# Performance work log

Measured on AMD Instinct MI355X. Metric: run time of the kernel, lower is better.

Reference implementation:

```python
import jax, jax.numpy as jnp
import numpy as np

B, N, D_IN, D_OUT, H = 4, 512, 1024, 1024, 16
HD = D_IN // H      # key head dim (FAISS k_features)
VD = D_OUT // H     # value head dim
MEM = 32768         # memory_size per head
IPQ = 8             # items_per_query
SCALE = HD ** -0.5


def setup_inputs() -> dict:
    key = jax.random.key(0)
    ks = jax.random.split(key, 9)
    s = 0.02
    return {
        "x": jax.random.normal(ks[0], (B, N, D_IN), jnp.float32),
        "Wq": jax.random.normal(ks[1], (D_IN, D_IN), jnp.float32) * s,
        "Wk": jax.random.normal(ks[2], (D_IN, D_IN), jnp.float32) * s,
        "Wv": jax.random.normal(ks[3], (D_OUT, D_IN), jnp.float32) * s,
        "Ww": jax.random.normal(ks[4], (D_OUT, D_IN), jnp.float32) * s,
        "Wo": jax.random.normal(ks[5], (D_OUT, D_OUT), jnp.float32) * s,
        "bo": jnp.zeros((D_OUT,), jnp.float32),
        "k_mem0": jax.random.normal(ks[6], (H, MEM, HD), jnp.float32) * s,
        "v_mem0": jax.random.normal(ks[7], (H, MEM, VD), jnp.float32) * s,
    }


def _attention(q, k, v, Wo, bo):
    # q: [b,n,D_IN], k: [b,m,D_IN], v: [b,m,D_OUT]
    b, n, _ = q.shape
    m = k.shape[1]
    qh = q.reshape(b, n, H, HD)
    kh = k.reshape(b, m, H, HD)
    vh = v.reshape(b, m, H, VD)
    sim = jnp.einsum("bihd,bjhd->bhij", qh, kh) * SCALE
    att = jax.nn.softmax(sim, axis=-1)
    out = jnp.einsum("bhij,bjhd->bihd", att, vh).reshape(b, n, H * VD)
    return out @ Wo.T + bo


def reference(x, Wq, Wk, Wv, Ww, Wo, bo, k_mem0, v_mem0):
    b, n, _ = x.shape
    q = x @ Wq.T          # [b,n,D_IN]
    k = x @ Wk.T          # [b,n,D_IN]
    v = x @ Wv.T          # [b,n,D_OUT]
    w = jax.nn.sigmoid(x @ Ww.T)

    a = _attention(q, k, v, Wo, bo)

    # per-head flat views: [h, b*n, hd]
    qh = q.reshape(b, n, H, HD).transpose(2, 0, 1, 3).reshape(H, b * n, HD)
    kh = k.reshape(b, n, H, HD).transpose(2, 0, 1, 3).reshape(H, b * n, HD)
    vh = v.reshape(b, n, H, VD).transpose(2, 0, 1, 3).reshape(H, b * n, VD)

    m_ins = b * n
    # FIFO insert: drop oldest m_ins rows, append new keys/values
    k_mem = jnp.concatenate([k_mem0[:, m_ins:], kh], axis=1)  # [h, MEM, HD]
    v_mem = jnp.concatenate([v_mem0[:, m_ins:], vh], axis=1)  # [h, MEM, VD]

    # exact inner-product search (IndexFlatIP), top IPQ per query, per head
    sims = jnp.einsum("hqd,hmd->hqm", qh, k_mem)               # [h, b*n, MEM]
    _, idx = jax.lax.top_k(sims, IPQ)                          # [h, b*n, IPQ]
    idx = idx.reshape(H, b * n * IPQ, 1)
    k_ret = jnp.take_along_axis(k_mem, idx, axis=1)            # [h, b*n*IPQ, HD]
    v_ret = jnp.take_along_axis(v_mem, idx, axis=1)            # [h, b*n*IPQ, VD]

    # 'h (b m) hd -> b m (h hd)' with m = n*IPQ
    k_m = k_ret.reshape(H, b, n * IPQ, HD).transpose(1, 2, 0, 3).reshape(b, n * IPQ, D_IN)
    v_m = v_ret.reshape(H, b, n * IPQ, VD).transpose(1, 2, 0, 3).reshape(b, n * IPQ, D_OUT)

    a_m = _attention(q, k_m, v_m, Wo, bo)
    return w * a + (1.0 - w) * a_m
```

## Files before the change

### kernel.cpp

```cpp
#include <hip/hip_runtime.h>
#include <float.h>
#include <math.h>


#define DIN   1024
#define NHEADS 16
#define HD    64
#define NB    4
#define NSEQ  512
#define BN    2048
#define MEMN  32768
#define OLDN  30720
#define IPQ   8
#define ATT_SCALE 0.125f
#define SZ    (BN * DIN)

typedef __attribute__((ext_vector_type(4))) float floatx4;
typedef __attribute__((ext_vector_type(8))) short short8;

__device__ __forceinline__ unsigned short f2bf(float f) {
    unsigned int u = __float_as_uint(f);
    return (unsigned short)((u + 0x7FFFu + ((u >> 16) & 1u)) >> 16);
}
__device__ __forceinline__ float bf2f(unsigned short s) {
    return __uint_as_float(((unsigned int)s) << 16);
}
__device__ __forceinline__ void split_pack(float4 a, float4 b, short8 &hi, short8 &lo) {
    float vals[8] = {a.x, a.y, a.z, a.w, b.x, b.y, b.z, b.w};
#pragma unroll
    for (int j = 0; j < 8; ++j) {
        unsigned short h = f2bf(vals[j]);
        hi[j] = (short)h;
        lo[j] = (short)f2bf(vals[j] - bf2f(h));
    }
}
__device__ __forceinline__ floatx4 mfma16(short8 a, short8 b, floatx4 c) {
    return __builtin_amdgcn_mfma_f32_16x16x32_bf16(a, b, c, 0, 0, 0);
}

__global__ void init_kernel(unsigned int* nrm) {
    if (threadIdx.x < NHEADS) nrm[threadIdx.x] = 0u;
}

__global__ __launch_bounds__(256) void gemm_mfma(
    const float* __restrict__ A,
    const float* __restrict__ W0, const float* __restrict__ W1,
    const float* __restrict__ W2, const float* __restrict__ W3,
    float* __restrict__ C0, float* __restrict__ C1,
    float* __restrict__ C2, float* __restrict__ C3,
    int sigmoidZ)
{
    __shared__ short Ahi_s[128 * 32];
    __shared__ short Alo_s[128 * 32];
    __shared__ short Bhi_s[128 * 32];
    __shared__ short Blo_s[128 * 32];

    int z = blockIdx.z;
    const float* W = (z == 0) ? W0 : (z == 1) ? W1 : (z == 2) ? W2 : W3;
    float* C = (z == 0) ? C0 : (z == 1) ? C1 : (z == 2) ? C2 : C3;

    int tid = threadIdx.x;
    int wv = tid >> 6, lane = tid & 63, quad = lane >> 4, l16 = lane & 15;
    int row0 = blockIdx.y * 128, col0 = blockIdx.x * 128;
    int wm = (wv >> 1) * 64, wn = (wv & 1) * 64;

    floatx4 zero4 = {0.f, 0.f, 0.f, 0.f};
    floatx4 acc[4][4];
#pragma unroll
    for (int i = 0; i < 4; ++i)
#pragma unroll
        for (int j = 0; j < 4; ++j) acc[i][j] = zero4;

    for (int kk = 0; kk < DIN; kk += 32) {
        __syncthreads();
#pragma unroll
        for (int p = 0; p < 2; ++p) {
            int g = tid * 2 + p;
            int row = g >> 2, cc = (g & 3) * 8;
            const float* ap = A + (size_t)(row0 + row) * DIN + kk + cc;
            float4 a0 = *(const float4*)ap;
            float4 a1 = *(const float4*)(ap + 4);
            short8 h8, l8;
            split_pack(a0, a1, h8, l8);
            *(short8*)&Ahi_s[g * 8] = h8;
            *(short8*)&Alo_s[g * 8] = l8;
            const float* bp = W + (size_t)(col0 + row) * DIN + kk + cc;
            float4 b0 = *(const float4*)bp;
            float4 b1 = *(const float4*)(bp + 4);
            split_pack(b0, b1, h8, l8);
            *(short8*)&Bhi_s[g * 8] = h8;
            *(short8*)&Blo_s[g * 8] = l8;
        }
        __syncthreads();

        short8 ah[4], al[4], bh[4], bl[4];
#pragma unroll
        for (int t = 0; t < 4; ++t) {
            int ar = (wm + t * 16 + l16) * 32 + quad * 8;
            int br = (wn + t * 16 + l16) * 32 + quad * 8;
            ah[t] = *(const short8*)&Ahi_s[ar];
            al[t] = *(const short8*)&Alo_s[ar];
            bh[t] = *(const short8*)&Bhi_s[br];
            bl[t] = *(const short8*)&Blo_s[br];
        }
#pragma unroll
        for (int tm = 0; tm < 4; ++tm)
#pragma unroll
            for (int tn = 0; tn < 4; ++tn) {
                floatx4 c = acc[tm][tn];
                c = mfma16(al[tm], bl[tn], c);
                c = mfma16(al[tm], bh[tn], c);
                c = mfma16(ah[tm], bl[tn], c);
                c = mfma16(ah[tm], bh[tn], c);
                acc[tm][tn] = c;
            }
    }

    bool sig = (sigmoidZ == z);
#pragma unroll
    for (int tm = 0; tm < 4; ++tm)
#pragma unroll
        for (int tn = 0; tn < 4; ++tn)
#pragma unroll
            for (int r = 0; r < 4; ++r) {
                int row = row0 + wm + tm * 16 + quad * 4 + r;
                int col = col0 + wn + tn * 16 + l16;
                float vv = acc[tm][tn][r];
                if (sig) vv = 1.f / (1.f + __expf(-vv));
                C[(size_t)row * DIN + col] = vv;
            }
}

__global__ __launch_bounds__(256) void oldnorm_kernel(
    const float* __restrict__ kmem0, unsigned int* __restrict__ nrm)
{
    int h = blockIdx.y;
    int c0 = blockIdx.x * 1024;
    int part = threadIdx.x & 15, rg = threadIdx.x >> 4;
    const float* base = kmem0 + ((size_t)h * MEMN + BN) * HD;
    float mx = 0.f;
    for (int it = 0; it < 64; ++it) {
        int row = c0 + it * 16 + rg;
        float4 vv = *(const float4*)(base + (size_t)row * HD + part * 4);
        float s = vv.x * vv.x + vv.y * vv.y + vv.z * vv.z + vv.w * vv.w;
#pragma unroll
        for (int o = 1; o < 16; o <<= 1) s += __shfl_xor(s, o, 16);
        mx = fmaxf(mx, s);
    }
    __shared__ float red[256];
    red[threadIdx.x] = mx;
    __syncthreads();
    for (int st = 128; st > 0; st >>= 1) {
        if (threadIdx.x < st) red[threadIdx.x] = fmaxf(red[threadIdx.x], red[threadIdx.x + st]);
        __syncthreads();
    }
    if (threadIdx.x == 0) atomicMax(nrm + h, __float_as_uint(sqrtf(red[0])));
}

__device__ __forceinline__ void insert_top8(float (&tv)[8], int (&ti)[8], float v, int id) {
    if (v < tv[7] || (v == tv[7] && id > ti[7])) return;
    tv[7] = v; ti[7] = id;
#pragma unroll
    for (int s = 7; s > 0; --s) {
        bool sw = (tv[s] > tv[s - 1]) || (tv[s] == tv[s - 1] && ti[s] < ti[s - 1]);
        if (sw) {
            float fv = tv[s]; tv[s] = tv[s - 1]; tv[s - 1] = fv;
            int iv = ti[s]; ti[s] = ti[s - 1]; ti[s - 1] = iv;
        }
    }
}

__global__ __launch_bounds__(256, 2) void search_kernel(
    const float* __restrict__ q, const float* __restrict__ knew,
    const float* __restrict__ kmem0, const unsigned int* __restrict__ nrm,
    int* __restrict__ idxOut)
{
    __shared__ short Khi[32 * 72];
    __shared__ short Klo[32 * 72];
    __shared__ int sflag;
    int tid = threadIdx.x;
    int qt = blockIdx.x, h = blockIdx.y;
    int wv = tid >> 6, lane = tid & 63, quad = lane >> 4, l16 = lane & 15;
    if (tid == 0) sflag = 0;

    short8 qhi[2], qlo[2];
    float qn2;
    {
        int qrow = qt * 64 + wv * 16 + l16;
        const float* qp = q + (size_t)qrow * DIN + h * HD;
        float sq = 0.f;
#pragma unroll
        for (int st = 0; st < 2; ++st) {
            float4 a = *(const float4*)(qp + st * 32 + quad * 8);
            float4 c = *(const float4*)(qp + st * 32 + quad * 8 + 4);
            sq += a.x * a.x + a.y * a.y + a.z * a.z + a.w * a.w
                + c.x * c.x + c.y * c.y + c.z * c.z + c.w * c.w;
            split_pack(a, c, qhi[st], qlo[st]);
        }
        sq += __shfl_xor(sq, 16);
        sq += __shfl_xor(sq, 32);
        qn2 = sq;
    }

    float tv[4][8]; int ti[4][8];
#pragma unroll
    for (int r = 0; r < 4; ++r)
#pragma unroll
        for (int s = 0; s < 8; ++s) { tv[r][s] = -FLT_MAX; ti[r][s] = 0x7FFFFFFF; }

    for (int ch = 0; ch < 64; ++ch) {
        __syncthreads();
        {
            int key = tid >> 3, part = tid & 7;
            const float* kr = knew + (size_t)(ch * 32 + key) * DIN + h * HD;
            float4 ka = *(const float4*)(kr + part * 8);
            float4 kb = *(const float4*)(kr + part * 8 + 4);
            short8 kh8, kl8;
            split_pack(ka, kb, kh8, kl8);
            *(short8*)&Khi[key * 72 + part * 8] = kh8;
            *(short8*)&Klo[key * 72 + part * 8] = kl8;
        }
        __syncthreads();

        short8 kh00 = *(const short8*)&Khi[l16 * 72 + quad * 8];
        short8 kh01 = *(const short8*)&Khi[l16 * 72 + 32 + quad * 8];
        short8 kl00 = *(const short8*)&Klo[l16 * 72 + quad * 8];
        short8 kl01 = *(const short8*)&Klo[l16 * 72 + 32 + quad * 8];
        short8 kh10 = *(const short8*)&Khi[(16 + l16) * 72 + quad * 8];
        short8 kh11 = *(const short8*)&Khi[(16 + l16) * 72 + 32 + quad * 8];
        short8 kl10 = *(const short8*)&Klo[(16 + l16) * 72 + quad * 8];
        short8 kl11 = *(const short8*)&Klo[(16 + l16) * 72 + 32 + quad * 8];
        floatx4 zero4 = {0.f, 0.f, 0.f, 0.f};
        floatx4 s0 = zero4, s1 = zero4;
        s0 = mfma16(qhi[0], kh00, s0); s0 = mfma16(qhi[1], kh01, s0);
        s0 = mfma16(qlo[0], kh00, s0); s0 = mfma16(qlo[1], kh01, s0);
        s0 = mfma16(qhi[0], kl00, s0); s0 = mfma16(qhi[1], kl01, s0);
        s1 = mfma16(qhi[0], kh10, s1); s1 = mfma16(qhi[1], kh11, s1);
        s1 = mfma16(qlo[0], kh10, s1); s1 = mfma16(qlo[1], kh11, s1);
        s1 = mfma16(qhi[0], kl10, s1); s1 = mfma16(qhi[1], kl11, s1);

        int base = OLDN + ch * 32;
#pragma unroll
        for (int r = 0; r < 4; ++r) {
            insert_top8(tv[r], ti[r], s0[r], base + l16);
            insert_top8(tv[r], ti[r], s1[r], base + 16 + l16);
        }
    }

    float val8[4], keepv[4];
    int keepi[4];
#pragma unroll
    for (int rr = 0; rr < 4; ++rr) { keepv[rr] = -FLT_MAX; keepi[rr] = 0x7FFFFFFF; val8[rr] = -FLT_MAX; }
#pragma unroll
    for (int rr = 0; rr < 4; ++rr) {
#pragma unroll
        for (int m = 0; m < 8; ++m) {
            float cv = tv[rr][0]; int ci = ti[rr][0];
#pragma unroll
            for (int o = 1; o < 16; o <<= 1) {
                float ov = __shfl_xor(cv, o, 16);
                int oi = __shfl_xor(ci, o, 16);
                if (ov > cv || (ov == cv && oi < ci)) { cv = ov; ci = oi; }
            }
            if (tv[rr][0] == cv && ti[rr][0] == ci) {
#pragma unroll
                for (int s = 0; s < 7; ++s) { tv[rr][s] = tv[rr][s + 1]; ti[rr][s] = ti[rr][s + 1]; }
                tv[rr][7] = -FLT_MAX; ti[rr][7] = 0x7FFFFFFF;
            }
            if (l16 == m) { keepv[rr] = cv; keepi[rr] = ci; }
            if (l16 == 0)
                idxOut[((size_t)h * BN + qt * 64 + wv * 16 + quad * 4 + rr) * IPQ + m] = ci;
            val8[rr] = cv;
        }
    }

    float oldMax = __uint_as_float(nrm[h]);
    bool need = false;
#pragma unroll
    for (int rr = 0; rr < 4; ++rr) {
        float bq = __shfl(qn2, quad * 4 + rr, 16);
        float bnd = sqrtf(bq) * oldMax * 1.0001f + 1e-5f;
        if (bnd >= val8[rr]) need = true;
    }
    if (need) sflag = 1;
    __syncthreads();

    if (sflag) {
#pragma unroll
        for (int rr = 0; rr < 4; ++rr) {
            tv[rr][0] = (l16 < 8) ? keepv[rr] : -FLT_MAX;
            ti[rr][0] = (l16 < 8) ? keepi[rr] : 0x7FFFFFFF;
#pragma unroll
            for (int s = 1; s < 8; ++s) { tv[rr][s] = -FLT_MAX; ti[rr][s] = 0x7FFFFFFF; }
        }
        for (int ch = 0; ch < 960; ++ch) {
            __syncthreads();
            {
                int key = tid >> 3, part = tid & 7;
                const float* kr = kmem0 + ((size_t)h * MEMN + BN + ch * 32 + key) * HD;
                float4 ka = *(const float4*)(kr + part * 8);
                float4 kb = *(const float4*)(kr + part * 8 + 4);
                short8 kh8, kl8;
                split_pack(ka, kb, kh8, kl8);
                *(short8*)&Khi[key * 72 + part * 8] = kh8;
                *(short8*)&Klo[key * 72 + part * 8] = kl8;
            }
            __syncthreads();

            short8 kh00 = *(const short8*)&Khi[l16 * 72 + quad * 8];
            short8 kh01 = *(const short8*)&Khi[l16 * 72 + 32 + quad * 8];
            short8 kl00 = *(const short8*)&Klo[l16 * 72 + quad * 8];
            short8 kl01 = *(const short8*)&Klo[l16 * 72 + 32 + quad * 8];
            short8 kh10 = *(const short8*)&Khi[(16 + l16) * 72 + quad * 8];
            short8 kh11 = *(const short8*)&Khi[(16 + l16) * 72 + 32 + quad * 8];
            short8 kl10 = *(const short8*)&Klo[(16 + l16) * 72 + quad * 8];
            short8 kl11 = *(const short8*)&Klo[(16 + l16) * 72 + 32 + quad * 8];
            floatx4 zero4 = {0.f, 0.f, 0.f, 0.f};
            floatx4 s0 = zero4, s1 = zero4;
            s0 = mfma16(qhi[0], kh00, s0); s0 = mfma16(qhi[1], kh01, s0);
            s0 = mfma16(qlo[0], kh00, s0); s0 = mfma16(qlo[1], kh01, s0);
            s0 = mfma16(qhi[0], kl00, s0); s0 = mfma16(qhi[1], kl01, s0);
            s1 = mfma16(qhi[0], kh10, s1); s1 = mfma16(qhi[1], kh11, s1);
            s1 = mfma16(qlo[0], kh10, s1); s1 = mfma16(qlo[1], kh11, s1);
            s1 = mfma16(qhi[0], kl10, s1); s1 = mfma16(qhi[1], kl11, s1);

            int base = ch * 32;
#pragma unroll
            for (int r = 0; r < 4; ++r) {
                insert_top8(tv[r], ti[r], s0[r], base + l16);
                insert_top8(tv[r], ti[r], s1[r], base + 16 + l16);
            }
        }
#pragma unroll
        for (int rr = 0; rr < 4; ++rr) {
#pragma unroll
            for (int m = 0; m < 8; ++m) {
                float cv = tv[rr][0]; int ci = ti[rr][0];
#pragma unroll
                for (int o = 1; o < 16; o <<= 1) {
                    float ov = __shfl_xor(cv, o, 16);
                    int oi = __shfl_xor(ci, o, 16);
                    if (ov > cv || (ov == cv && oi < ci)) { cv = ov; ci = oi; }
                }
                if (tv[rr][0] == cv && ti[rr][0] == ci) {
#pragma unroll
                    for (int s = 0; s < 7; ++s) { tv[rr][s] = tv[rr][s + 1]; ti[rr][s] = ti[rr][s + 1]; }
                    tv[rr][7] = -FLT_MAX; ti[rr][7] = 0x7FFFFFFF;
                }
                if (l16 == 0)
                    idxOut[((size_t)h * BN + qt * 64 + wv * 16 + quad * 4 + rr) * IPQ + m] = ci;
            }
        }
    }
}

__global__ __launch_bounds__(256, 2) void attn_kernel(
    const float* __restrict__ q, const float* __restrict__ knew,
    const float* __restrict__ vnew, const float* __restrict__ kmem0,
    const float* __restrict__ vmem0, const int* __restrict__ idxb,
    float* __restrict__ outp, int gatherMode, int nkeys)
{
    __shared__ short Khi[32 * 72];
    __shared__ short Klo[32 * 72];
    __shared__ short Vthi[64 * 40];
    __shared__ short Vtlo[64 * 40];
    __shared__ short Pbuf[4 * 16 * 40];
    int tid = threadIdx.x;
    int qt = blockIdx.x, h = blockIdx.y, b = blockIdx.z;
    int wv = tid >> 6, lane = tid & 63, quad = lane >> 4, l16 = lane & 15;

    short8 qhi[2], qlo[2];
    {
        int qrow = b * NSEQ + qt * 64 + wv * 16 + l16;
        const float* qp = q + (size_t)qrow * DIN + h * HD;
#pragma unroll
        for (int st = 0; st < 2; ++st) {
            float4 a = *(const float4*)(qp + st * 32 + quad * 8);
            float4 c = *(const float4*)(qp + st * 32 + quad * 8 + 4);
            split_pack(a, c, qhi[st], qlo[st]);
        }
    }
    floatx4 zero4 = {0.f, 0.f, 0.f, 0.f};
    floatx4 Oacc[4];
#pragma unroll
    for (int t = 0; t < 4; ++t) Oacc[t] = zero4;
    float mrow[4], lrow[4];
#pragma unroll
    for (int r = 0; r < 4; ++r) { mrow[r] = -3.0e38f; lrow[r] = 0.f; }

    int nch = nkeys >> 5;
    for (int ch = 0; ch < nch; ++ch) {
        __syncthreads();
        {
            int key = tid >> 3, part = tid & 7;
            const float *kr, *vr;
            if (!gatherMode) {
                int row = b * NSEQ + ch * 32 + key;
                kr = knew + (size_t)row * DIN + h * HD;
                vr = vnew + (size_t)row * DIN + h * HD;
            } else {
                int J = ch * 32 + key;
                int mi = idxb[((size_t)h * BN + b * NSEQ + (J >> 3)) * IPQ + (J & 7)];
                if (mi < OLDN) {
                    kr = kmem0 + ((size_t)h * MEMN + BN + mi) * HD;
                    vr = vmem0 + ((size_t)h * MEMN + BN + mi) * HD;
                } else {
                    kr = knew + (size_t)(mi - OLDN) * DIN + h * HD;
                    vr = vnew + (size_t)(mi - OLDN) * DIN + h * HD;
                }
            }
            float4 ka = *(const float4*)(kr + part * 8);
            float4 kb = *(const float4*)(kr + part * 8 + 4);
            short8 kh8, kl8;
            split_pack(ka, kb, kh8, kl8);
            *(short8*)&Khi[key * 72 + part * 8] = kh8;
            *(short8*)&Klo[key * 72 + part * 8] = kl8;
            float4 va = *(const float4*)(vr + part * 8);
            float4 vb = *(const float4*)(vr + part * 8 + 4);
            float vals[8] = {va.x, va.y, va.z, va.w, vb.x, vb.y, vb.z, vb.w};
#pragma unroll
            for (int u = 0; u < 8; ++u) {
                int d = part * 8 + u;
                unsigned short hh = f2bf(vals[u]);
                Vthi[d * 40 + key] = (short)hh;
                Vtlo[d * 40 + key] = (short)f2bf(vals[u] - bf2f(hh));
            }
        }
        __syncthreads();

        short8 kh00 = *(const short8*)&Khi[(l16) * 72 + 0 * 32 + quad * 8];
        short8 kh01 = *(const short8*)&Khi[(l16) * 72 + 1 * 32 + quad * 8];
        short8 kl00 = *(const short8*)&Klo[(l16) * 72 + 0 * 32 + quad * 8];
        short8 kl01 = *(const short8*)&Klo[(l16) * 72 + 1 * 32 + quad * 8];
        short8 kh10 = *(const short8*)&Khi[(16 + l16) * 72 + 0 * 32 + quad * 8];
        short8 kh11 = *(const short8*)&Khi[(16 + l16) * 72 + 1 * 32 + quad * 8];
        short8 kl10 = *(const short8*)&Klo[(16 + l16) * 72 + 0 * 32 + quad * 8];
        short8 kl11 = *(const short8*)&Klo[(16 + l16) * 72 + 1 * 32 + quad * 8];
        floatx4 s0 = zero4, s1 = zero4;
        s0 = mfma16(qhi[0], kh00, s0); s0 = mfma16(qhi[1], kh01, s0);
        s0 = mfma16(qlo[0], kh00, s0); s0 = mfma16(qlo[1], kh01, s0);
        s0 = mfma16(qhi[0], kl00, s0); s0 = mfma16(qhi[1], kl01, s0);
        s1 = mfma16(qhi[0], kh10, s1); s1 = mfma16(qhi[1], kh11, s1);
        s1 = mfma16(qlo[0], kh10, s1); s1 = mfma16(qlo[1], kh11, s1);
        s1 = mfma16(qhi[0], kl10, s1); s1 = mfma16(qhi[1], kl11, s1);

        float cm[4], alpha[4], p0[4], p1[4], rs[4];
#pragma unroll
        for (int r = 0; r < 4; ++r) cm[r] = fmaxf(s0[r], s1[r]) * ATT_SCALE;
#pragma unroll
        for (int o = 1; o < 16; o <<= 1) {
#pragma unroll
            for (int r = 0; r < 4; ++r) cm[r] = fmaxf(cm[r], __shfl_xor(cm[r], o, 16));
        }
#pragma unroll
        for (int r = 0; r < 4; ++r) {
            float mn = fmaxf(mrow[r], cm[r]);
            alpha[r] = __expf(mrow[r] - mn);
            p0[r] = __expf(s0[r] * ATT_SCALE - mn);
            p1[r] = __expf(s1[r] * ATT_SCALE - mn);
            mrow[r] = mn;
            rs[r] = p0[r] + p1[r];
        }
#pragma unroll
        for (int o = 1; o < 16; o <<= 1) {
#pragma unroll
            for (int r = 0; r < 4; ++r) rs[r] += __shfl_xor(rs[r], o, 16);
        }
#pragma unroll
        for (int r = 0; r < 4; ++r) {
            lrow[r] = lrow[r] * alpha[r] + rs[r];
            Pbuf[(wv * 16 + quad * 4 + r) * 40 + l16] = (short)f2bf(p0[r]);
            Pbuf[(wv * 16 + quad * 4 + r) * 40 + 16 + l16] = (short)f2bf(p1[r]);
        }
#pragma unroll
        for (int t = 0; t < 4; ++t)
#pragma unroll
            for (int r = 0; r < 4; ++r) Oacc[t][r] *= alpha[r];
        __syncthreads();

        short8 pf = *(const short8*)&Pbuf[(wv * 16 + l16) * 40 + quad * 8];
#pragma unroll
        for (int t = 0; t < 4; ++t) {
            short8 vh = *(const short8*)&Vthi[(t * 16 + l16) * 40 + quad * 8];
            short8 vl = *(const short8*)&Vtlo[(t * 16 + l16) * 40 + quad * 8];
            floatx4 o = Oacc[t];
            o = mfma16(pf, vh, o);
            o = mfma16(pf, vl, o);
            Oacc[t] = o;
        }
    }
#pragma unroll
    for (int t = 0; t < 4; ++t)
#pragma unroll
        for (int r = 0; r < 4; ++r) {
            int qrow = b * NSEQ + qt * 64 + wv * 16 + quad * 4 + r;
            outp[(size_t)qrow * DIN + h * HD + t * 16 + l16] = Oacc[t][r] / lrow[r];
        }
}

__global__ __launch_bounds__(256) void combine_kernel(
    const float* __restrict__ G, const float* __restrict__ wg,
    const float* __restrict__ bo, float* __restrict__ out)
{
    int gid = blockIdx.x * 256 + threadIdx.x;
    float4 g1 = ((const float4*)G)[gid];
    float4 g2 = ((const float4*)G)[gid + (SZ / 4)];
    float4 w4 = ((const float4*)wg)[gid];
    float4 b4 = ((const float4*)bo)[gid & (DIN / 4 - 1)];
    float4 o;
    o.x = w4.x * g1.x + (1.f - w4.x) * g2.x + b4.x;
    o.y = w4.y * g1.y + (1.f - w4.y) * g2.y + b4.y;
    o.z = w4.z * g1.z + (1.f - w4.z) * g2.z + b4.z;
    o.w = w4.w * g1.w + (1.f - w4.w) * g2.w + b4.w;
    ((float4*)out)[gid] = o;
}

extern "C" void kernel_launch(void* const* d_in, const int* in_sizes, int n_in,
                              void* d_out, int out_size, void* d_ws, size_t ws_size,
                              hipStream_t stream)
{
    (void)in_sizes; (void)n_in; (void)out_size; (void)ws_size;
    const float* x     = (const float*)d_in[0];
    const float* Wq    = (const float*)d_in[1];
    const float* Wk    = (const float*)d_in[2];
    const float* Wv    = (const float*)d_in[3];
    const float* Ww    = (const float*)d_in[4];
    const float* Wo    = (const float*)d_in[5];
    const float* bo    = (const float*)d_in[6];
    const float* kmem0 = (const float*)d_in[7];
    const float* vmem0 = (const float*)d_in[8];

    float* ws = (float*)d_ws;
    float* q  = ws;
    float* k  = ws + (size_t)SZ;
    float* v  = ws + (size_t)2 * SZ;
    float* wg = ws + (size_t)3 * SZ;
    float* AO = ws + (size_t)4 * SZ;
    float* G  = ws + (size_t)6 * SZ;
    int* idxb = (int*)(ws + (size_t)8 * SZ);
    unsigned int* nrm = (unsigned int*)(ws + (size_t)8 * SZ + NHEADS * BN * IPQ);

    init_kernel<<<1, 64, 0, stream>>>(nrm);
    gemm_mfma<<<dim3(8, 16, 4), 256, 0, stream>>>(x, Wq, Wk, Wv, Ww, q, k, v, wg, 3);
    oldnorm_kernel<<<dim3(30, 16), 256, 0, stream>>>(kmem0, nrm);
    search_kernel<<<dim3(32, 16), 256, 0, stream>>>(q, k, kmem0, nrm, idxb);
    attn_kernel<<<dim3(8, 16, 4), 256, 0, stream>>>(q, k, v, kmem0, vmem0, idxb, AO, 0, 512);
    attn_kernel<<<dim3(8, 16, 4), 256, 0, stream>>>(q, k, v, kmem0, vmem0, idxb,
                                                    AO + (size_t)SZ, 1, 4096);
    gemm_mfma<<<dim3(8, 32, 1), 256, 0, stream>>>(AO, Wo, Wo, Wo, Wo, G, G, G, G, -1);
    combine_kernel<<<2048, 256, 0, stream>>>(G, wg, bo, (float*)d_out);
}
```

Before: 1.081 ms.

## Prefetch next K/V chunk into registers and swizzle transposed V in LDS

The attention kernel now issues the global loads for the next 32-key chunk right after writing the current chunk to shared memory, so load latency overlaps with the MFMA and softmax work. Transposed V stores use an XOR-swizzled column to cut LDS bank conflicts, with matching reads. One of the three block barriers is removed and the others use raw s_barrier with an explicit lgkmcnt wait. The grid is remapped so head/batch pairs are the fastest-varying block index. Dropping the barrier before the P·V step relies on each wave reading only its own Pbuf rows, and the prefetch raises register pressure.

```diff
diff --git a/kernel.cpp b/kernel.cpp
--- a/kernel.cpp
+++ b/kernel.cpp
@@ -366,7 +366,8 @@
     __shared__ short Vtlo[64 * 40];
     __shared__ short Pbuf[4 * 16 * 40];
     int tid = threadIdx.x;
-    int qt = blockIdx.x, h = blockIdx.y, b = blockIdx.z;
+    int pair = blockIdx.x, qt = blockIdx.y;
+    int h = pair >> 2, b = pair & 3;
     int wv = tid >> 6, lane = tid & 63, quad = lane >> 4, l16 = lane & 15;
 
     short8 qhi[2], qlo[2];
@@ -388,45 +389,56 @@
 #pragma unroll
     for (int r = 0; r < 4; ++r) { mrow[r] = -3.0e38f; lrow[r] = 0.f; }
 
+    int key = tid >> 3, part = tid & 7;
+    int vcol = (((key >> 3) ^ (part & 3)) << 3) | (key & 7);
+    float4 ka, kb, va, vb;
+    auto gload = [&](int chl) {
+        const float *kr, *vr;
+        if (!gatherMode) {
+            int row = b * NSEQ + chl * 32 + key;
+            kr = knew + (size_t)row * DIN + h * HD;
+            vr = vnew + (size_t)row * DIN + h * HD;
+        } else {
+            int J = chl * 32 + key;
+            int mi = idxb[((size_t)h * BN + b * NSEQ + (J >> 3)) * IPQ + (J & 7)];
+            if (mi < OLDN) {
+                kr = kmem0 + ((size_t)h * MEMN + BN + mi) * HD;
+                vr = vmem0 + ((size_t)h * MEMN + BN + mi) * HD;
+            } else {
+                kr = knew + (size_t)(mi - OLDN) * DIN + h * HD;
+                vr = vnew + (size_t)(mi - OLDN) * DIN + h * HD;
+            }
+        }
+        ka = *(const float4*)(kr + part * 8);
+        kb = *(const float4*)(kr + part * 8 + 4);
+        va = *(const float4*)(vr + part * 8);
+        vb = *(const float4*)(vr + part * 8 + 4);
+    };
+
     int nch = nkeys >> 5;
+    gload(0);
     for (int ch = 0; ch < nch; ++ch) {
-        __syncthreads();
+        asm volatile("s_waitcnt lgkmcnt(0)" ::: "memory");
+        __builtin_amdgcn_s_barrier();
+
         {
-            int key = tid >> 3, part = tid & 7;
-            const float *kr, *vr;
-            if (!gatherMode) {
-                int row = b * NSEQ + ch * 32 + key;
-                kr = knew + (size_t)row * DIN + h * HD;
-                vr = vnew + (size_t)row * DIN + h * HD;
-            } else {
-                int J = ch * 32 + key;
-                int mi = idxb[((size_t)h * BN + b * NSEQ + (J >> 3)) * IPQ + (J & 7)];
-                if (mi < OLDN) {
-                    kr = kmem0 + ((size_t)h * MEMN + BN + mi) * HD;
-                    vr = vmem0 + ((size_t)h * MEMN + BN + mi) * HD;
-                } else {
-                    kr = knew + (size_t)(mi - OLDN) * DIN + h * HD;
-                    vr = vnew + (size_t)(mi - OLDN) * DIN + h * HD;
-                }
-            }
-            float4 ka = *(const float4*)(kr + part * 8);
-            float4 kb = *(const float4*)(kr + part * 8 + 4);
             short8 kh8, kl8;
             split_pack(ka, kb, kh8, kl8);
             *(short8*)&Khi[key * 72 + part * 8] = kh8;
             *(short8*)&Klo[key * 72 + part * 8] = kl8;
-            float4 va = *(const float4*)(vr + part * 8);
-            float4 vb = *(const float4*)(vr + part * 8 + 4);
             float vals[8] = {va.x, va.y, va.z, va.w, vb.x, vb.y, vb.z, vb.w};
 #pragma unroll
             for (int u = 0; u < 8; ++u) {
                 int d = part * 8 + u;
                 unsigned short hh = f2bf(vals[u]);
-                Vthi[d * 40 + key] = (short)hh;
-                Vtlo[d * 40 + key] = (short)f2bf(vals[u] - bf2f(hh));
-            }
-        }
-        __syncthreads();
+                Vthi[d * 40 + vcol] = (short)hh;
+                Vtlo[d * 40 + vcol] = (short)f2bf(vals[u] - bf2f(hh));
+            }
+        }
+        if (ch + 1 < nch) gload(ch + 1);
+
+        asm volatile("s_waitcnt lgkmcnt(0)" ::: "memory");
+        __builtin_amdgcn_s_barrier();
 
         short8 kh00 = *(const short8*)&Khi[(l16) * 72 + 0 * 32 + quad * 8];
         short8 kh01 = *(const short8*)&Khi[(l16) * 72 + 1 * 32 + quad * 8];
@@ -476,13 +488,14 @@
         for (int t = 0; t < 4; ++t)
 #pragma unroll
             for (int r = 0; r < 4; ++r) Oacc[t][r] *= alpha[r];
-        __syncthreads();
 
         short8 pf = *(const short8*)&Pbuf[(wv * 16 + l16) * 40 + quad * 8];
 #pragma unroll
         for (int t = 0; t < 4; ++t) {
-            short8 vh = *(const short8*)&Vthi[(t * 16 + l16) * 40 + quad * 8];
-            short8 vl = *(const short8*)&Vtlo[(t * 16 + l16) * 40 + quad * 8];
+            int dd = t * 16 + l16;
+            int vc = ((quad ^ ((dd >> 3) & 3)) << 3);
+            short8 vh = *(const short8*)&Vthi[dd * 40 + vc];
+            short8 vl = *(const short8*)&Vtlo[dd * 40 + vc];
             floatx4 o = Oacc[t];
             o = mfma16(pf, vh, o);
             o = mfma16(pf, vl, o);
@@ -544,8 +557,8 @@
     gemm_mfma<<<dim3(8, 16, 4), 256, 0, stream>>>(x, Wq, Wk, Wv, Ww, q, k, v, wg, 3);
     oldnorm_kernel<<<dim3(30, 16), 256, 0, stream>>>(kmem0, nrm);
     search_kernel<<<dim3(32, 16), 256, 0, stream>>>(q, k, kmem0, nrm, idxb);
-    attn_kernel<<<dim3(8, 16, 4), 256, 0, stream>>>(q, k, v, kmem0, vmem0, idxb, AO, 0, 512);
-    attn_kernel<<<dim3(8, 16, 4), 256, 0, stream>>>(q, k, v, kmem0, vmem0, idxb,
+    attn_kernel<<<dim3(64, 8, 1), 256, 0, stream>>>(q, k, v, kmem0, vmem0, idxb, AO, 0, 512);
+    attn_kernel<<<dim3(64, 8, 1), 256, 0, stream>>>(q, k, v, kmem0, vmem0, idxb,
                                                     AO + (size_t)SZ, 1, 4096);
     gemm_mfma<<<dim3(8, 32, 1), 256, 0, stream>>>(AO, Wo, Wo, Wo, Wo, G, G, G, G, -1);
     combine_kernel<<<2048, 256, 0, stream>>>(G, wg, bo, (float*)d_out);
```

Result: faster. 998.3 us (-7.7%).
